# Kernel optimization log

Measured on AMD Instinct MI355X. Metric: run time of the kernel, lower is better.

The kernel has to match this reference:

```python
import jax, jax.numpy as jnp
import numpy as np

B, D, K, U = 4096, 1024, 5, 1024  # batch, input_dim, num_basis, units


def setup_inputs() -> dict:
    key = jax.random.key(0)
    k1, k2, k3 = jax.random.split(key, 3)
    x = jax.random.normal(k1, (B, D), dtype=jnp.float32)
    basis_weights = jax.random.normal(k2, (D, K, U), dtype=jnp.float32) * 0.02
    bias = jax.random.normal(k3, (U,), dtype=jnp.float32) * 0.02
    return {"x": x, "basis_weights": basis_weights, "bias": bias}


def reference(x, basis_weights, bias):
    # Polynomial basis expansion: x^0, x^1, ..., x^{K-1}  -> (B, D, K)
    num_basis = basis_weights.shape[1]
    powers = jnp.arange(num_basis, dtype=x.dtype)
    basis = x[..., None] ** powers  # x**0 == 1, matching tf.ones_like branch
    # Fused: einsum('bik,ikj->bij') followed by reduce_sum over i == 'bik,ikj->bj'.
    # Avoids materializing the (B, D, U) intermediate of the original.
    out = jnp.einsum("bik,ikj->bj", basis, basis_weights) + bias
    # tf.nn.gelu defaults to exact (non-approximate) GELU.
    return jax.nn.gelu(out, approximate=False)
```

## Files before the change

kernel.cpp:

```cpp
#include <hip/hip_runtime.h>
#include <hip/hip_bf16.h>
#include <math.h>


#define B_DIM 4096
#define D_DIM 1024
#define U_DIM 1024
#define KT2 4096
#define NKB 128

typedef unsigned short ushort_t;
typedef __attribute__((ext_vector_type(8))) short bf16x8;
typedef __attribute__((ext_vector_type(4))) float f32x4;

__device__ __forceinline__ ushort_t f2bf(float f) {
  union { float f; unsigned int u; } v;
  v.f = f;
  unsigned int r = v.u + 0x7FFFu + ((v.u >> 16) & 1u);
  return (ushort_t)(r >> 16);
}

__device__ __forceinline__ void load_lds16(const ushort_t* g, ushort_t* l) {
  __builtin_amdgcn_global_load_lds(
      (const __attribute__((address_space(1))) ushort_t*)g,
      (__attribute__((address_space(3))) ushort_t*)l, 16, 0, 0);
}

__device__ __forceinline__ float gelu_exact(float v) {
  return 0.5f * v * (1.0f + erff(v * 0.70710678118654752f));
}


__global__ __launch_bounds__(256) void basis_pack_kernel(
    const float* __restrict__ x, ushort_t* __restrict__ Ap,
    float* __restrict__ fold) {
  if (blockIdx.x == 0 && blockIdx.y == 0) {
#pragma unroll
    for (int q = 0; q < 4; ++q) fold[q * 256 + threadIdx.x] = 0.0f;
  }
  const int t    = threadIdx.x;
  const int wave = t >> 6;
  const int lane = t & 63;
  const int kblk = blockIdx.x * 4 + wave;
  const int m16  = blockIdx.y;
  const int m    = lane & 15;
  const int ko   = lane >> 4;
  const int row  = m16 * 16 + m;
  const int i0   = kblk * 8 + ko * 2;

  const float xa = x[(size_t)row * D_DIM + i0];
  const float xb = x[(size_t)row * D_DIM + i0 + 1];
  const float xa2 = xa * xa, xb2 = xb * xb;
  ushort_t o[8];
  o[0] = f2bf(xa);  o[1] = f2bf(xa2); o[2] = f2bf(xa2 * xa); o[3] = f2bf(xa2 * xa2);
  o[4] = f2bf(xb);  o[5] = f2bf(xb2); o[6] = f2bf(xb2 * xb); o[7] = f2bf(xb2 * xb2);
  *(uint4*)(Ap + ((size_t)m16 * NKB + kblk) * 512 + lane * 8) = *(const uint4*)o;
}

__global__ __launch_bounds__(256) void w_pack_kernel(
    const float* __restrict__ W, ushort_t* __restrict__ Bp,
    float* __restrict__ fold) {
  const int t    = threadIdx.x;
  const int wave = t >> 6;
  const int lane = t & 63;
  const int kblk = blockIdx.x * 4 + wave;
  const int n16  = blockIdx.y;
  const int jj   = lane & 15;
  const int ko   = lane >> 4;
  const int j    = n16 * 16 + jj;
  const int i0   = kblk * 8 + ko * 2;

  ushort_t o[8];
  float s0 = 0.0f;
#pragma unroll
  for (int t2 = 0; t2 < 2; ++t2) {
    const int i = i0 + t2;
    s0 += W[(size_t)(i * 5) * U_DIM + j];
#pragma unroll
    for (int e = 0; e < 4; ++e) {
      const int r = i * 5 + e + 1;
      o[t2 * 4 + e] = f2bf(W[(size_t)r * U_DIM + j]);
    }
  }
  *(uint4*)(Bp + ((size_t)n16 * NKB + kblk) * 512 + lane * 8) = *(const uint4*)o;
  s0 += __shfl_xor(s0, 16, 64);
  s0 += __shfl_xor(s0, 32, 64);
  if (ko == 0) atomicAdd(&fold[j], s0);
}

__global__ __launch_bounds__(256) void gemm_kernel(
    const ushort_t* __restrict__ Ap, const ushort_t* __restrict__ Bp,
    const float* __restrict__ bias, const float* __restrict__ fold,
    float* __restrict__ C) {
  __shared__ __align__(16) ushort_t lds[4][12 * 512];

  const int tid  = threadIdx.x;
  const int wave = tid >> 6;
  const int lane = tid & 63;
  const int wm   = wave >> 1;
  const int wn   = wave & 1;

  const int lin  = blockIdx.y * 8 + blockIdx.x;
  const int xcd  = lin & 7;
  const int slot = lin >> 3;
  const int mt   = xcd * 8 + (slot & 7);
  const int nt   = slot >> 3;
  const int m16b = mt * 4;
  const int n16b = nt * 8;

  const ushort_t* gcur[3];
  int ldst[3];
#pragma unroll
  for (int s = 0; s < 3; ++s) {
    const int u = s * 4 + wave;
    const ushort_t* base = (u < 4)
        ? Ap + ((size_t)(m16b + u) * NKB) * 512
        : Bp + ((size_t)(n16b + (u - 4)) * NKB) * 512;
    gcur[s] = base + lane * 8;
    ldst[s] = u * 512 + lane * 8;
  }

  f32x4 acc[2][4];
  const f32x4 zero = {0.0f, 0.0f, 0.0f, 0.0f};
#pragma unroll
  for (int mf = 0; mf < 2; ++mf)
#pragma unroll
    for (int nf = 0; nf < 4; ++nf) acc[mf][nf] = zero;

#define WAITBAR(N) \
  asm volatile("s_waitcnt vmcnt(" #N ")\n\ts_barrier" ::: "memory")

#define STAGE_REL(bb, rel)                                              \
  do {                                                                  \
    _Pragma("unroll")                                                   \
    for (int s = 0; s < 3; ++s)                                         \
      load_lds16(gcur[s] + (rel) * 512, &lds[bb][ldst[s]]);             \
  } while (0)

#define COMPUTE(bb)                                                     \
  do {                                                                  \
    bf16x8 a[2], b[4];                                                  \
    _Pragma("unroll")                                                   \
    for (int mf = 0; mf < 2; ++mf)                                      \
      a[mf] = *(const bf16x8*)&lds[bb][(wm * 2 + mf) * 512 + lane * 8]; \
    _Pragma("unroll")                                                   \
    for (int nf = 0; nf < 4; ++nf)                                      \
      b[nf] = *(const bf16x8*)&lds[bb][(4 + wn * 4 + nf) * 512 + lane * 8]; \
    _Pragma("unroll")                                                   \
    for (int mf = 0; mf < 2; ++mf)                                      \
      _Pragma("unroll")                                                 \
      for (int nf = 0; nf < 4; ++nf)                                    \
        acc[mf][nf] = __builtin_amdgcn_mfma_f32_16x16x32_bf16(          \
            a[mf], b[nf], acc[mf][nf], 0, 0, 0);                        \
  } while (0)

  STAGE_REL(0, 0);
  STAGE_REL(1, 1);
  STAGE_REL(2, 2);
#pragma unroll
  for (int s = 0; s < 3; ++s) gcur[s] += 4 * 512;

  for (int base = 0; base < 124; base += 4) {
    WAITBAR(6); STAGE_REL(3, -1); COMPUTE(0);
    WAITBAR(6); STAGE_REL(0,  0); COMPUTE(1);
    WAITBAR(6); STAGE_REL(1,  1); COMPUTE(2);
    WAITBAR(6); STAGE_REL(2,  2); COMPUTE(3);
#pragma unroll
    for (int s = 0; s < 3; ++s) gcur[s] += 4 * 512;
  }
  WAITBAR(6); STAGE_REL(3, -1); COMPUTE(0);
  WAITBAR(6); COMPUTE(1);
  WAITBAR(3); COMPUTE(2);
  WAITBAR(0); COMPUTE(3);
#undef STAGE_REL
#undef COMPUTE
#undef WAITBAR

  const int crow0 = m16b * 16 + wm * 32 + (lane >> 4) * 4;
  const int ccol0 = n16b * 16 + wn * 64 + (lane & 15);
#pragma unroll
  for (int nf = 0; nf < 4; ++nf) {
    const int col = ccol0 + nf * 16;
    const float bv = bias[col] + fold[col];
#pragma unroll
    for (int mf = 0; mf < 2; ++mf) {
#pragma unroll
      for (int r = 0; r < 4; ++r) {
        const int row = crow0 + mf * 16 + r;
        C[(size_t)row * U_DIM + col] = gelu_exact(acc[mf][nf][r] + bv);
      }
    }
  }
}

__global__ void fallback_kernel(const float* __restrict__ x, const float* __restrict__ W,
                                const float* __restrict__ bias, float* __restrict__ out) {
  int j  = blockIdx.x * 256 + threadIdx.x;
  int b0 = blockIdx.y * 16;
  float acc[16];
#pragma unroll
  for (int t = 0; t < 16; ++t) acc[t] = 0.0f;
  for (int i = 0; i < D_DIM; ++i) {
    const float* wr = W + (size_t)i * 5 * U_DIM + j;
    float w0 = wr[0 * U_DIM], w1 = wr[1 * U_DIM], w2 = wr[2 * U_DIM];
    float w3 = wr[3 * U_DIM], w4 = wr[4 * U_DIM];
#pragma unroll
    for (int t = 0; t < 16; ++t) {
      float xv = x[(size_t)(b0 + t) * D_DIM + i];
      float x2 = xv * xv;
      acc[t] += w0 + xv * w1 + x2 * w2 + x2 * xv * w3 + x2 * x2 * w4;
    }
  }
  float bv = bias[j];
#pragma unroll
  for (int t = 0; t < 16; ++t)
    out[(size_t)(b0 + t) * U_DIM + j] = gelu_exact(acc[t] + bv);
}

extern "C" void kernel_launch(void* const* d_in, const int* in_sizes, int n_in,
                              void* d_out, int out_size, void* d_ws, size_t ws_size,
                              hipStream_t stream) {
  const float* x    = (const float*)d_in[0];
  const float* W    = (const float*)d_in[1];
  const float* bias = (const float*)d_in[2];
  float* out = (float*)d_out;

  const size_t szA = (size_t)B_DIM * KT2 * sizeof(ushort_t);
  const size_t szB = (size_t)U_DIM * KT2 * sizeof(ushort_t);
  const size_t szF = (size_t)U_DIM * sizeof(float);

  if (ws_size >= szA + szB + szF) {
    ushort_t* Ap   = (ushort_t*)d_ws;
    ushort_t* Bp   = (ushort_t*)((char*)d_ws + szA);
    float*    fld  = (float*)((char*)d_ws + szA + szB);
    basis_pack_kernel<<<dim3(NKB / 4, B_DIM / 16), 256, 0, stream>>>(x, Ap, fld);
    w_pack_kernel<<<dim3(NKB / 4, U_DIM / 16), 256, 0, stream>>>(W, Bp, fld);
    gemm_kernel<<<dim3(U_DIM / 128, B_DIM / 64), 256, 0, stream>>>(Ap, Bp, bias, fld, out);
  } else {
    fallback_kernel<<<dim3(U_DIM / 256, B_DIM / 16), 256, 0, stream>>>(x, W, bias, out);
  }
}
```

Measured before the change: 137.1 us.

## Merge basis and weight packing into one prep kernel with deterministic bias fold

Replaces the two packing kernels with a single prep kernel. Its first 1024 blocks stage x rows through LDS with coalesced float4 loads, then emit the bf16 polynomial basis. The last 64 blocks each pack one 16-column strip of W across all k-blocks and reduce the x^0 column sum in LDS, writing bias+fold directly. This saves a launch, the fold zeroing and the global atomics. The cost is long serial loops in the 64 weight blocks, which may become a tail on the critical path.

```diff
diff --git a/kernel.cpp b/kernel.cpp
--- a/kernel.cpp
+++ b/kernel.cpp
@@ -31,67 +31,79 @@
 }
 
 
-__global__ __launch_bounds__(256) void basis_pack_kernel(
-    const float* __restrict__ x, ushort_t* __restrict__ Ap,
-    float* __restrict__ fold) {
-  if (blockIdx.x == 0 && blockIdx.y == 0) {
-#pragma unroll
-    for (int q = 0; q < 4; ++q) fold[q * 256 + threadIdx.x] = 0.0f;
-  }
+__global__ __launch_bounds__(256) void prep_kernel(
+    const float* __restrict__ x, const float* __restrict__ W,
+    const float* __restrict__ bias, ushort_t* __restrict__ Ap,
+    ushort_t* __restrict__ Bp, float* __restrict__ b2) {
+  __shared__ __align__(16) float lsh[16][260];
+
+  const int bid  = blockIdx.x;
   const int t    = threadIdx.x;
   const int wave = t >> 6;
   const int lane = t & 63;
-  const int kblk = blockIdx.x * 4 + wave;
-  const int m16  = blockIdx.y;
   const int m    = lane & 15;
   const int ko   = lane >> 4;
-  const int row  = m16 * 16 + m;
-  const int i0   = kblk * 8 + ko * 2;
-
-  const float xa = x[(size_t)row * D_DIM + i0];
-  const float xb = x[(size_t)row * D_DIM + i0 + 1];
-  const float xa2 = xa * xa, xb2 = xb * xb;
-  ushort_t o[8];
-  o[0] = f2bf(xa);  o[1] = f2bf(xa2); o[2] = f2bf(xa2 * xa); o[3] = f2bf(xa2 * xa2);
-  o[4] = f2bf(xb);  o[5] = f2bf(xb2); o[6] = f2bf(xb2 * xb); o[7] = f2bf(xb2 * xb2);
-  *(uint4*)(Ap + ((size_t)m16 * NKB + kblk) * 512 + lane * 8) = *(const uint4*)o;
-}
-
-__global__ __launch_bounds__(256) void w_pack_kernel(
-    const float* __restrict__ W, ushort_t* __restrict__ Bp,
-    float* __restrict__ fold) {
-  const int t    = threadIdx.x;
-  const int wave = t >> 6;
-  const int lane = t & 63;
-  const int kblk = blockIdx.x * 4 + wave;
-  const int n16  = blockIdx.y;
-  const int jj   = lane & 15;
-  const int ko   = lane >> 4;
-  const int j    = n16 * 16 + jj;
-  const int i0   = kblk * 8 + ko * 2;
-
-  ushort_t o[8];
-  float s0 = 0.0f;
-#pragma unroll
-  for (int t2 = 0; t2 < 2; ++t2) {
-    const int i = i0 + t2;
-    s0 += W[(size_t)(i * 5) * U_DIM + j];
-#pragma unroll
-    for (int e = 0; e < 4; ++e) {
-      const int r = i * 5 + e + 1;
-      o[t2 * 4 + e] = f2bf(W[(size_t)r * U_DIM + j]);
-    }
-  }
-  *(uint4*)(Bp + ((size_t)n16 * NKB + kblk) * 512 + lane * 8) = *(const uint4*)o;
-  s0 += __shfl_xor(s0, 16, 64);
-  s0 += __shfl_xor(s0, 32, 64);
-  if (ko == 0) atomicAdd(&fold[j], s0);
+
+  if (bid < 1024) {
+    const int bx  = bid & 3;
+    const int m16 = bid >> 2;
+    const float* xbase = x + (size_t)m16 * 16 * D_DIM + bx * 256;
+#pragma unroll
+    for (int p = 0; p < 4; ++p) {
+      const int row = p * 4 + wave;
+      const int c4  = lane;
+      *(float4*)&lsh[row][c4 * 4] =
+          *(const float4*)(xbase + (size_t)row * D_DIM + c4 * 4);
+    }
+    __syncthreads();
+#pragma unroll
+    for (int u = 0; u < 8; ++u) {
+      const int kl  = u * 4 + wave;
+      const int col = kl * 8 + ko * 2;
+      const float xa = lsh[m][col], xb = lsh[m][col + 1];
+      const float xa2 = xa * xa, xb2 = xb * xb;
+      ushort_t o[8];
+      o[0] = f2bf(xa);  o[1] = f2bf(xa2);
+      o[2] = f2bf(xa2 * xa); o[3] = f2bf(xa2 * xa2);
+      o[4] = f2bf(xb);  o[5] = f2bf(xb2);
+      o[6] = f2bf(xb2 * xb); o[7] = f2bf(xb2 * xb2);
+      *(uint4*)(Ap + ((size_t)m16 * NKB + bx * 32 + kl) * 512 + lane * 8) =
+          *(const uint4*)o;
+    }
+  } else {
+    const int n16 = bid - 1024;
+    const int j   = n16 * 16 + m;
+    float s0 = 0.0f;
+#pragma unroll 2
+    for (int it2 = 0; it2 < 32; ++it2) {
+      const int kblk = it2 * 4 + wave;
+      const int i0   = kblk * 8 + ko * 2;
+      ushort_t o[8];
+#pragma unroll
+      for (int t2 = 0; t2 < 2; ++t2) {
+        const int i = i0 + t2;
+        s0 += W[(size_t)(i * 5) * U_DIM + j];
+#pragma unroll
+        for (int e = 0; e < 4; ++e)
+          o[t2 * 4 + e] = f2bf(W[(size_t)(i * 5 + e + 1) * U_DIM + j]);
+      }
+      *(uint4*)(Bp + ((size_t)n16 * NKB + kblk) * 512 + lane * 8) =
+          *(const uint4*)o;
+    }
+    s0 += __shfl_xor(s0, 16, 64);
+    s0 += __shfl_xor(s0, 32, 64);
+    float* red = &lsh[0][0];
+    __syncthreads();
+    if (ko == 0) red[wave * 16 + m] = s0;
+    __syncthreads();
+    if (wave == 0 && ko == 0)
+      b2[j] = bias[j] + red[m] + red[16 + m] + red[32 + m] + red[48 + m];
+  }
 }
 
 __global__ __launch_bounds__(256) void gemm_kernel(
     const ushort_t* __restrict__ Ap, const ushort_t* __restrict__ Bp,
-    const float* __restrict__ bias, const float* __restrict__ fold,
-    float* __restrict__ C) {
+    const float* __restrict__ b2, float* __restrict__ C) {
   __shared__ __align__(16) ushort_t lds[4][12 * 512];
 
   const int tid  = threadIdx.x;
@@ -181,7 +193,7 @@
 #pragma unroll
   for (int nf = 0; nf < 4; ++nf) {
     const int col = ccol0 + nf * 16;
-    const float bv = bias[col] + fold[col];
+    const float bv = b2[col];
 #pragma unroll
     for (int mf = 0; mf < 2; ++mf) {
 #pragma unroll
@@ -227,15 +239,14 @@
 
   const size_t szA = (size_t)B_DIM * KT2 * sizeof(ushort_t);
   const size_t szB = (size_t)U_DIM * KT2 * sizeof(ushort_t);
-  const size_t szF = (size_t)U_DIM * sizeof(float);
-
-  if (ws_size >= szA + szB + szF) {
-    ushort_t* Ap   = (ushort_t*)d_ws;
-    ushort_t* Bp   = (ushort_t*)((char*)d_ws + szA);
-    float*    fld  = (float*)((char*)d_ws + szA + szB);
-    basis_pack_kernel<<<dim3(NKB / 4, B_DIM / 16), 256, 0, stream>>>(x, Ap, fld);
-    w_pack_kernel<<<dim3(NKB / 4, U_DIM / 16), 256, 0, stream>>>(W, Bp, fld);
-    gemm_kernel<<<dim3(U_DIM / 128, B_DIM / 64), 256, 0, stream>>>(Ap, Bp, bias, fld, out);
+  const size_t szb = (size_t)U_DIM * sizeof(float);
+
+  if (ws_size >= szA + szB + szb) {
+    ushort_t* Ap = (ushort_t*)d_ws;
+    ushort_t* Bp = (ushort_t*)((char*)d_ws + szA);
+    float*    b2 = (float*)((char*)d_ws + szA + szB);
+    prep_kernel<<<dim3(1024 + 64), 256, 0, stream>>>(x, W, bias, Ap, Bp, b2);
+    gemm_kernel<<<dim3(U_DIM / 128, B_DIM / 64), 256, 0, stream>>>(Ap, Bp, b2, out);
   } else {
     fallback_kernel<<<dim3(U_DIM / 256, B_DIM / 16), 256, 0, stream>>>(x, W, bias, out);
   }
```

New measurement: 138.2 us. Within noise of the previous version (+0.9%).
